# Performance work log

Measured on AMD Instinct MI355X. Metric: run time of the kernel, lower is better.

## Reference

```python
import jax, jax.numpy as jnp
import numpy as np

D = 1024
H = 16
DH = D // H  # 64
EPS_LN = 1e-5
CONF_MIN = 1e-6


def sparsemax(z):
    """Sparsemax along the last axis (Martins & Astudillo 2016)."""
    K = z.shape[-1]
    z_sorted = jnp.flip(jnp.sort(z, axis=-1), axis=-1)          # descending
    cssv = jnp.cumsum(z_sorted, axis=-1)                        # cumulative sums
    r = jnp.arange(1, K + 1, dtype=z.dtype)                     # 1..K
    support = (1.0 + r * z_sorted) > cssv                       # bool mask
    k = jnp.sum(support, axis=-1, keepdims=True)                # support size
    tau = (jnp.take_along_axis(cssv, k.astype(jnp.int32) - 1, axis=-1) - 1.0) / k.astype(z.dtype)
    return jnp.maximum(z - tau, 0.0)


def setup_inputs() -> dict:
    key = jax.random.key(0)
    ks = jax.random.split(key, 16)
    B, P, K = 8, 512, 16
    s = 0.02
    return {
        "cell_query": jax.random.normal(ks[0], (B, D), jnp.float32),
        "gene_facets": jax.random.normal(ks[1], (B, P, K, D), jnp.float32),
        "confidence": jax.random.uniform(ks[2], (B, P, K), jnp.float32),
        "wq": jax.random.normal(ks[3], (D, D), jnp.float32) * s,
        "bq": jnp.zeros((D,), jnp.float32),
        "wk": jax.random.normal(ks[4], (D, D), jnp.float32) * s,
        "bk": jnp.zeros((D,), jnp.float32),
        "wv": jax.random.normal(ks[5], (D, D), jnp.float32) * s,
        "bv": jnp.zeros((D,), jnp.float32),
        "wo": jax.random.normal(ks[6], (D, D), jnp.float32) * s,
        "bo": jnp.zeros((D,), jnp.float32),
        "gamma": jnp.ones((D,), jnp.float32),
        "beta": jnp.zeros((D,), jnp.float32),
    }


def reference(cell_query, gene_facets, confidence,
              wq, bq, wk, bk, wv, bv, wo, bo, gamma, beta):
    B = gene_facets.shape[0]
    P = gene_facets.shape[1]
    Kf = gene_facets.shape[2]

    # Projections (torch Linear: x @ W^T + b; here weights stored already transposed as (D,D))
    Q = (cell_query @ wq + bq).reshape(B, H, DH)                       # (B,H,d)
    Kp = (gene_facets @ wk + bk).reshape(B, P, Kf, H, DH)              # (B,P,K,H,d)
    Vp = (gene_facets @ wv + bv).reshape(B, P, Kf, H, DH)              # (B,P,K,H,d)

    # scores: (B,P,H,K)
    scores = jnp.einsum('bhd,bpkhd->bphk', Q, Kp) / jnp.sqrt(jnp.asarray(DH, Q.dtype))
    conf_bias = jnp.log(jnp.clip(confidence, CONF_MIN))                # (B,P,K)
    scores = scores + conf_bias[:, :, None, :]

    alpha = sparsemax(scores)                                          # (B,P,H,K), dropout_p=0 -> identity

    out = jnp.einsum('bphk,bpkhd->bphd', alpha, Vp).reshape(B, P, D)
    out = out @ wo + bo

    # LayerNorm over last dim
    mu = jnp.mean(out, axis=-1, keepdims=True)
    var = jnp.mean((out - mu) ** 2, axis=-1, keepdims=True)
    out = (out - mu) * jax.lax.rsqrt(var + EPS_LN) * gamma + beta
    return out, alpha
```

## Files before the change

### kernel.cpp

```cpp
#include <hip/hip_runtime.h>


typedef float f32x4 __attribute__((ext_vector_type(4)));
typedef short s16x4 __attribute__((ext_vector_type(4)));
typedef short s16x8 __attribute__((ext_vector_type(8)));

__device__ __forceinline__ unsigned short f2bf(float f) {
  unsigned u = __builtin_bit_cast(unsigned, f);
  u = (u + 0x7FFFu + ((u >> 16) & 1u)) >> 16;
  return (unsigned short)u;
}

__device__ __forceinline__ float bf2f(unsigned short u) {
  return __builtin_bit_cast(float, ((unsigned)u) << 16);
}

__device__ __forceinline__ s16x8 pack8(s16x4 lo, s16x4 hi) {
  s16x8 r;
  r[0] = lo[0]; r[1] = lo[1]; r[2] = lo[2]; r[3] = lo[3];
  r[4] = hi[0]; r[5] = hi[1]; r[6] = hi[2]; r[7] = hi[3];
  return r;
}

__global__ __launch_bounds__(256) void k_transq(
    const float* __restrict__ wv, const float* __restrict__ wo,
    unsigned short* __restrict__ wvt, unsigned short* __restrict__ wot,
    const float* __restrict__ cq, const float* __restrict__ wq,
    float* __restrict__ qpart) {
  int bid = blockIdx.x;
  int t = threadIdx.x;
  if (bid < 512) {
    __shared__ float ts[64][65];
    const float* src = (bid < 256) ? wv : wo;
    unsigned short* dst = (bid < 256) ? wvt : wot;
    int tile = bid & 255;
    int er = (tile >> 4) << 6;
    int cb = (tile & 15) << 6;
    int r = t >> 2, c0 = (t & 3) << 4;
#pragma unroll
    for (int j = 0; j < 16; j += 4) {
      f32x4 v = *(const f32x4*)&src[(long)(er + r) * 1024 + cb + c0 + j];
      ts[r][c0 + j + 0] = v[0];
      ts[r][c0 + j + 1] = v[1];
      ts[r][c0 + j + 2] = v[2];
      ts[r][c0 + j + 3] = v[3];
    }
    __syncthreads();
    s16x8 o0, o1;
#pragma unroll
    for (int j = 0; j < 8; ++j) o0[j] = (short)f2bf(ts[c0 + j][r]);
#pragma unroll
    for (int j = 0; j < 8; ++j) o1[j] = (short)f2bf(ts[c0 + 8 + j][r]);
    long ob = (long)(cb + r) * 1024 + er + c0;
    *(s16x8*)&dst[ob] = o0;
    *(s16x8*)&dst[ob + 8] = o1;
  } else {
    int idx = bid - 512;
    int eq = idx >> 2, dq = idx & 3;
    int d = (dq << 8) + t;
    float acc[8] = {};
    for (int i = 0; i < 64; ++i) {
      int e = (eq << 6) + i;
      float w = wq[(long)e * 1024 + d];
#pragma unroll
      for (int b = 0; b < 8; ++b) acc[b] += w * cq[(b << 10) + e];
    }
#pragma unroll
    for (int b = 0; b < 8; ++b)
      qpart[(long)((b << 4) + eq) * 1024 + d] = acc[b];
  }
}

__global__ __launch_bounds__(256) void k_wtilde(
    const float* __restrict__ wk, const float* __restrict__ bk,
    const float* __restrict__ bq, const float* __restrict__ qpart,
    unsigned short* __restrict__ wt, float* __restrict__ cvec) {
  __shared__ float Qs[16][68];
  int et = blockIdx.x, b = blockIdx.y, t = threadIdx.x;
  {
    int d0 = t << 2;
    f32x4 s4 = *(const f32x4*)&bq[d0];
#pragma unroll
    for (int q = 0; q < 16; ++q)
      s4 += *(const f32x4*)&qpart[(long)((b << 4) + q) * 1024 + d0];
    *(f32x4*)&Qs[d0 >> 6][d0 & 63] = s4;
  }
  __syncthreads();
  int h = t & 15, el = t >> 4;
#pragma unroll
  for (int ii = 0; ii < 2; ++ii) {
    int e = (et << 5) + (ii << 4) + el;
    const float* wr = &wk[(long)e * 1024 + (h << 6)];
    float s = 0.f;
#pragma unroll
    for (int d = 0; d < 64; d += 4) {
      f32x4 w = *(const f32x4*)&wr[d];
      s += w[0] * Qs[h][d] + w[1] * Qs[h][d + 1] + w[2] * Qs[h][d + 2] + w[3] * Qs[h][d + 3];
    }
    wt[(long)((b << 4) + h) * 1024 + e] = f2bf(s);
  }
  if (et == 0 && t < 16) {
    float s = 0.f;
    for (int d = 0; d < 64; ++d) s += bk[(t << 6) + d] * Qs[t][d];
    cvec[(b << 4) + t] = s;
  }
}

#define GSTR 1028
#define TSTR 20
__global__ __launch_bounds__(256, 2) void k_scores(
    const float* __restrict__ G, const float* __restrict__ conf,
    const unsigned short* __restrict__ wt, const float* __restrict__ cvec,
    float* __restrict__ alpha_out, unsigned short* __restrict__ gbar,
    int b0, int hstride) {
  __shared__ short Gs[16 * GSTR];
  __shared__ short Gt[1024 * TSTR];
  __shared__ short As[16 * 32];
  __shared__ float ps[1024];
  __shared__ float lc[16];

  int t = threadIdx.x;
  int lane = t & 63, w = t >> 6;
  int l15 = lane & 15, g4 = lane >> 4;
  int bp = blockIdx.x;
  long gbp = (long)b0 * 512 + bp;
  int b = (int)(gbp >> 9);
  const float* Grow = G + gbp * 16384;
  const unsigned short* wtb = wt + (long)b * 16384;

#pragma unroll
  for (int half = 0; half < 2; ++half) {
    s16x4 col[8];
#pragma unroll
    for (int j = 0; j < 8; ++j) {
      int k = (half << 3) + j;
      f32x4 g = *(const f32x4*)&Grow[(k << 10) + (t << 2)];
      s16x4 h4;
      h4[0] = (short)f2bf(g[0]); h4[1] = (short)f2bf(g[1]);
      h4[2] = (short)f2bf(g[2]); h4[3] = (short)f2bf(g[3]);
      *(s16x4*)&Gs[k * GSTR + (t << 2)] = h4;
      col[j] = h4;
    }
#pragma unroll
    for (int q = 0; q < 4; ++q) {
      int e = (t << 2) + q;
      s16x4 lo, hi;
      lo[0] = col[0][q]; lo[1] = col[1][q]; lo[2] = col[2][q]; lo[3] = col[3][q];
      hi[0] = col[4][q]; hi[1] = col[5][q]; hi[2] = col[6][q]; hi[3] = col[7][q];
      *(s16x4*)&Gt[e * TSTR + (half << 3)] = lo;
      *(s16x4*)&Gt[e * TSTR + (half << 3) + 4] = hi;
    }
  }
  if (t < 16) lc[t] = logf(fmaxf(conf[gbp * 16 + t], 1e-6f));
  __syncthreads();

  f32x4 sc = {0.f, 0.f, 0.f, 0.f};
#pragma unroll
  for (int i = 0; i < 8; ++i) {
    int e0 = (w << 8) + (i << 5) + (g4 << 3);
    s16x8 af = *(const s16x8*)&wtb[l15 * 1024 + e0];
    int off = l15 * GSTR + e0;
    s16x8 bf = pack8(*(const s16x4*)&Gs[off], *(const s16x4*)&Gs[off + 4]);
    sc = __builtin_amdgcn_mfma_f32_16x16x32_bf16(af, bf, sc, 0, 0, 0);
  }
#pragma unroll
  for (int r = 0; r < 4; ++r)
    ps[(w << 8) + ((g4 << 2) + r) * 16 + l15] = sc[r];
  __syncthreads();

  {
    int h = t >> 4, k = t & 15;
    float z = (ps[h * 16 + k] + ps[256 + h * 16 + k] + ps[512 + h * 16 + k] +
               ps[768 + h * 16 + k] + cvec[b * 16 + h]) * 0.125f + lc[k];
    float v = z;
#pragma unroll
    for (int kk = 2; kk <= 16; kk <<= 1) {
#pragma unroll
      for (int j = kk >> 1; j > 0; j >>= 1) {
        float o = __shfl_xor(v, j, 64);
        bool dirDesc = ((l15 & kk) == 0);
        bool takeMax = (((l15 & j) == 0) == dirDesc);
        v = takeMax ? fmaxf(v, o) : fminf(v, o);
      }
    }
    float cs = v;
#pragma unroll
    for (int d = 1; d < 16; d <<= 1) {
      float o = __shfl_up(cs, (unsigned)d, 16);
      if (l15 >= d) cs += o;
    }
    bool sup = (1.0f + (float)(l15 + 1) * v) > cs;
    unsigned long long m = __ballot(sup);
    int gb16 = lane & 48;
    int ksup = (int)__popcll((m >> gb16) & 0xFFFFull);
    float csk = __shfl(cs, ksup - 1, 16);
    float tau = (csk - 1.0f) / (float)ksup;
    float a = fmaxf(z - tau, 0.0f);
    alpha_out[((gbp << 4) + h) * 16 + k] = a;
    As[(h << 5) + k] = (short)f2bf(a);
    As[(h << 5) + 16 + k] = 0;
  }
  __syncthreads();

  s16x8 ab = *(const s16x8*)&As[(l15 << 5) + (g4 << 3)];
#pragma unroll 4
  for (int i = 0; i < 16; ++i) {
    int ebase = ((w << 4) + i) << 4;
    int ro = (ebase + l15) * TSTR + ((g4 & 1) << 3);
    s16x8 aa = pack8(*(const s16x4*)&Gt[ro], *(const s16x4*)&Gt[ro + 4]);
    f32x4 d2 = __builtin_amdgcn_mfma_f32_16x16x32_bf16(
        aa, ab, (f32x4){0.f, 0.f, 0.f, 0.f}, 0, 0, 0);
    s16x4 o4;
    o4[0] = (short)f2bf(d2[0]); o4[1] = (short)f2bf(d2[1]);
    o4[2] = (short)f2bf(d2[2]); o4[3] = (short)f2bf(d2[3]);
    *(s16x4*)&gbar[(long)l15 * hstride + (long)bp * 1024 + ebase + (g4 << 2)] = o4;
  }
}

__global__ __launch_bounds__(256) void k_av(
    const unsigned short* __restrict__ gbar, const unsigned short* __restrict__ wvt,
    const float* __restrict__ bv, unsigned short* __restrict__ av,
    int b0, int hstride) {
  __shared__ short Asm[64 * 40];
  __shared__ short Bsm[64 * 40];
  int t = threadIdx.x;
  int lane = t & 63, w = t >> 6;
  int l15 = lane & 15, g4 = lane >> 4;
  int wm = w >> 1, wn = w & 1;
  int tile = blockIdx.x, h = blockIdx.y;
  const unsigned short* Ab = gbar + (long)h * hstride + (long)tile * 64 * 1024;
  const unsigned short* Bb = wvt + (long)(h << 6) * 1024;
  int lr = t >> 2, lc = (t & 3) << 3;
  const unsigned short* Arp = Ab + (long)lr * 1024 + lc;
  const unsigned short* Brp = Bb + (long)lr * 1024 + lc;
  s16x8 a8 = *(const s16x8*)&Arp[0];
  s16x8 b8 = *(const s16x8*)&Brp[0];
  f32x4 acc[2][2] = {};
  for (int kb = 0; kb < 32; ++kb) {
    __syncthreads();
    *(s16x8*)&Asm[lr * 40 + lc] = a8;
    *(s16x8*)&Bsm[lr * 40 + lc] = b8;
    if (kb + 1 < 32) {
      a8 = *(const s16x8*)&Arp[((kb + 1) << 5)];
      b8 = *(const s16x8*)&Brp[((kb + 1) << 5)];
    }
    __syncthreads();
    s16x8 afr[2], bfr[2];
#pragma unroll
    for (int im = 0; im < 2; ++im)
      afr[im] = *(const s16x8*)&Asm[(wm * 32 + im * 16 + l15) * 40 + (g4 << 3)];
#pragma unroll
    for (int in = 0; in < 2; ++in)
      bfr[in] = *(const s16x8*)&Bsm[(wn * 32 + in * 16 + l15) * 40 + (g4 << 3)];
#pragma unroll
    for (int im = 0; im < 2; ++im)
#pragma unroll
      for (int in = 0; in < 2; ++in)
        acc[im][in] = __builtin_amdgcn_mfma_f32_16x16x32_bf16(afr[im], bfr[in], acc[im][in], 0, 0, 0);
  }
  long grow0 = (long)b0 * 512 + (long)tile * 64 + wm * 32 + (g4 << 2);
#pragma unroll
  for (int in = 0; in < 2; ++in) {
    int colg = (h << 6) + wn * 32 + in * 16 + l15;
    float bvv = bv[colg];
#pragma unroll
    for (int im = 0; im < 2; ++im) {
      long rowg = grow0 + im * 16;
#pragma unroll
      for (int r = 0; r < 4; ++r)
        av[(rowg + r) * 1024 + colg] = f2bf(acc[im][in][r] + bvv);
    }
  }
}

__global__ __launch_bounds__(256) void k_out(
    const unsigned short* __restrict__ av, const unsigned short* __restrict__ wot,
    const float* __restrict__ bo, unsigned short* __restrict__ yb) {
  __shared__ short Asm[64 * 40];
  __shared__ short Bsm[64 * 40];
  int mt = blockIdx.x, nt = blockIdx.y, t = threadIdx.x;
  int lane = t & 63, w = t >> 6;
  int wm = w >> 1, wn = w & 1;
  int l15 = lane & 15, g4 = lane >> 4;
  int lr = t >> 2, lc = (t & 3) << 3;
  const unsigned short* Arp = av + (long)(mt * 64 + lr) * 1024 + lc;
  const unsigned short* Brp = wot + (long)(nt * 64 + lr) * 1024 + lc;
  s16x8 a8 = *(const s16x8*)&Arp[0];
  s16x8 b8 = *(const s16x8*)&Brp[0];
  f32x4 acc[2][2] = {};
  for (int kb = 0; kb < 32; ++kb) {
    __syncthreads();
    *(s16x8*)&Asm[lr * 40 + lc] = a8;
    *(s16x8*)&Bsm[lr * 40 + lc] = b8;
    if (kb + 1 < 32) {
      a8 = *(const s16x8*)&Arp[((kb + 1) << 5)];
      b8 = *(const s16x8*)&Brp[((kb + 1) << 5)];
    }
    __syncthreads();
    s16x8 afr[2], bfr[2];
#pragma unroll
    for (int im = 0; im < 2; ++im)
      afr[im] = *(const s16x8*)&Asm[(wm * 32 + im * 16 + l15) * 40 + (g4 << 3)];
#pragma unroll
    for (int in = 0; in < 2; ++in)
      bfr[in] = *(const s16x8*)&Bsm[(wn * 32 + in * 16 + l15) * 40 + (g4 << 3)];
#pragma unroll
    for (int im = 0; im < 2; ++im)
#pragma unroll
      for (int in = 0; in < 2; ++in)
        acc[im][in] = __builtin_amdgcn_mfma_f32_16x16x32_bf16(afr[im], bfr[in], acc[im][in], 0, 0, 0);
  }
#pragma unroll
  for (int in = 0; in < 2; ++in) {
    int colg = nt * 64 + wn * 32 + in * 16 + l15;
    float bov = bo[colg];
#pragma unroll
    for (int im = 0; im < 2; ++im) {
      long rowg = (long)mt * 64 + wm * 32 + im * 16 + (g4 << 2);
#pragma unroll
      for (int r = 0; r < 4; ++r)
        yb[(rowg + r) * 1024 + colg] = f2bf(acc[im][in][r] + bov);
    }
  }
}

__global__ __launch_bounds__(256) void k_ln(
    const unsigned short* __restrict__ yb, const float* __restrict__ gamma,
    const float* __restrict__ beta, float* __restrict__ y) {
  int row = (blockIdx.x << 2) + (threadIdx.x >> 6);
  int lane = threadIdx.x & 63;
  const unsigned short* yr = yb + ((long)row << 10);
  float v[4][4];
  float s = 0.f, s2 = 0.f;
#pragma unroll
  for (int j = 0; j < 4; ++j) {
    s16x4 h4 = *(const s16x4*)&yr[(lane << 2) + (j << 8)];
#pragma unroll
    for (int q = 0; q < 4; ++q) {
      float f = bf2f((unsigned short)h4[q]);
      v[j][q] = f; s += f; s2 += f * f;
    }
  }
#pragma unroll
  for (int d = 1; d < 64; d <<= 1) {
    s += __shfl_xor(s, d, 64);
    s2 += __shfl_xor(s2, d, 64);
  }
  float mu = s * (1.0f / 1024.0f);
  float var = s2 * (1.0f / 1024.0f) - mu * mu;
  float rs = rsqrtf(var + 1e-5f);
  float* yo = y + ((long)row << 10);
#pragma unroll
  for (int j = 0; j < 4; ++j) {
    int f0 = (lane << 2) + (j << 8);
    f32x4 gm = *(const f32x4*)&gamma[f0];
    f32x4 bt = *(const f32x4*)&beta[f0];
    f32x4 o;
#pragma unroll
    for (int q = 0; q < 4; ++q) o[q] = (v[j][q] - mu) * rs * gm[q] + bt[q];
    *(f32x4*)&yo[f0] = o;
  }
}

extern "C" void kernel_launch(void* const* d_in, const int* in_sizes, int n_in,
                              void* d_out, int out_size, void* d_ws, size_t ws_size,
                              hipStream_t stream) {
  (void)in_sizes; (void)n_in; (void)out_size;
  const float* cq    = (const float*)d_in[0];
  const float* G     = (const float*)d_in[1];
  const float* conf  = (const float*)d_in[2];
  const float* wq    = (const float*)d_in[3];
  const float* bq    = (const float*)d_in[4];
  const float* wk    = (const float*)d_in[5];
  const float* bk    = (const float*)d_in[6];
  const float* wv    = (const float*)d_in[7];
  const float* bv    = (const float*)d_in[8];
  const float* wo    = (const float*)d_in[9];
  const float* bo    = (const float*)d_in[10];
  const float* gamma = (const float*)d_in[11];
  const float* beta  = (const float*)d_in[12];

  float* y = (float*)d_out;
  float* alpha = y + 4194304;

  char* p = (char*)d_ws;
  float* qpart = (float*)p;                  p += 8L * 16 * 1024 * 4;
  float* cvec  = (float*)p;                  p += 1024;
  unsigned short* wt   = (unsigned short*)p; p += 8L * 16 * 1024 * 2;
  unsigned short* wvt  = (unsigned short*)p; p += 1024L * 1024 * 2;
  unsigned short* wot  = (unsigned short*)p; p += 1024L * 1024 * 2;
  unsigned short* av   = (unsigned short*)p; p += 4096L * 1024 * 2;
  unsigned short* yb   = (unsigned short*)p; p += 4096L * 1024 * 2;
  unsigned short* gbar = (unsigned short*)p;
  size_t used = (size_t)(p - (char*)d_ws);
  size_t per_b = 512L * 16 * 1024 * 2;
  int nb = 1;
  if (ws_size >= used + 8 * per_b) nb = 8;
  else if (ws_size >= used + 4 * per_b) nb = 4;
  else if (ws_size >= used + 2 * per_b) nb = 2;
  int hstride = nb * 512 * 1024;

  hipLaunchKernelGGL(k_transq, dim3(576), dim3(256), 0, stream,
                     wv, wo, wvt, wot, cq, wq, qpart);
  hipLaunchKernelGGL(k_wtilde, dim3(32, 8), dim3(256), 0, stream, wk, bk, bq, qpart, wt, cvec);
  for (int c = 0; c < 8; c += nb) {
    hipLaunchKernelGGL(k_scores, dim3(nb * 512), dim3(256), 0, stream,
                       G, conf, wt, cvec, alpha, gbar, c, hstride);
    hipLaunchKernelGGL(k_av, dim3(nb * 8, 16), dim3(256), 0, stream,
                       gbar, wvt, bv, av, c, hstride);
  }
  hipLaunchKernelGGL(k_out, dim3(64, 16), dim3(256), 0, stream, av, wot, bo, yb);
  hipLaunchKernelGGL(k_ln, dim3(1024), dim3(256), 0, stream, yb, gamma, beta, y);
}
```

Baseline: 201.5 us.

## Stage gbar through LDS for coalesced stores, halve k_av tile, cap batch chunk at 4

k_scores now writes its per-head weighted facet sums into a shared-memory buffer (Gs) and then stores them to global memory as contiguous 16-byte vectors, replacing the scattered 8-byte per-lane stores. k_av uses 32-row M tiles instead of 64, which doubles its grid to give more blocks per launch. The batch chunk size is capped at 4, so the workspace footprint shrinks and there are two score/av launch pairs. The tradeoff is an extra LDS round trip and barrier in k_scores, less reuse per k_av block, and extra launches.

```diff
diff --git a/kernel.cpp b/kernel.cpp
--- a/kernel.cpp
+++ b/kernel.cpp
@@ -213,7 +213,18 @@
     s16x4 o4;
     o4[0] = (short)f2bf(d2[0]); o4[1] = (short)f2bf(d2[1]);
     o4[2] = (short)f2bf(d2[2]); o4[3] = (short)f2bf(d2[3]);
-    *(s16x4*)&gbar[(long)l15 * hstride + (long)bp * 1024 + ebase + (g4 << 2)] = o4;
+    *(s16x4*)&Gs[l15 * GSTR + ebase + (g4 << 2)] = o4;
+  }
+  __syncthreads();
+
+  unsigned short* gbo = gbar + (long)bp * 1024;
+#pragma unroll
+  for (int c2 = 0; c2 < 8; ++c2) {
+    int flat = (c2 << 11) + (t << 3);
+    int hh = flat >> 10, e = flat & 1023;
+    s16x4 lo = *(const s16x4*)&Gs[hh * GSTR + e];
+    s16x4 hi = *(const s16x4*)&Gs[hh * GSTR + e + 4];
+    *(s16x8*)&gbo[(long)hh * hstride + e] = pack8(lo, hi);
   }
 }
 
@@ -221,55 +232,48 @@
     const unsigned short* __restrict__ gbar, const unsigned short* __restrict__ wvt,
     const float* __restrict__ bv, unsigned short* __restrict__ av,
     int b0, int hstride) {
-  __shared__ short Asm[64 * 40];
+  __shared__ short Asm[32 * 40];
   __shared__ short Bsm[64 * 40];
   int t = threadIdx.x;
   int lane = t & 63, w = t >> 6;
   int l15 = lane & 15, g4 = lane >> 4;
   int wm = w >> 1, wn = w & 1;
   int tile = blockIdx.x, h = blockIdx.y;
-  const unsigned short* Ab = gbar + (long)h * hstride + (long)tile * 64 * 1024;
+  const unsigned short* Ab = gbar + (long)h * hstride + (long)tile * 32 * 1024;
   const unsigned short* Bb = wvt + (long)(h << 6) * 1024;
-  int lr = t >> 2, lc = (t & 3) << 3;
-  const unsigned short* Arp = Ab + (long)lr * 1024 + lc;
-  const unsigned short* Brp = Bb + (long)lr * 1024 + lc;
-  s16x8 a8 = *(const s16x8*)&Arp[0];
+  int ar = t >> 3, ac = (t & 7) << 2;
+  int br = t >> 2, bc = (t & 3) << 3;
+  const unsigned short* Arp = Ab + (long)ar * 1024 + ac;
+  const unsigned short* Brp = Bb + (long)br * 1024 + bc;
+  s16x4 a4 = *(const s16x4*)&Arp[0];
   s16x8 b8 = *(const s16x8*)&Brp[0];
-  f32x4 acc[2][2] = {};
+  f32x4 acc[2] = {};
   for (int kb = 0; kb < 32; ++kb) {
     __syncthreads();
-    *(s16x8*)&Asm[lr * 40 + lc] = a8;
-    *(s16x8*)&Bsm[lr * 40 + lc] = b8;
+    *(s16x4*)&Asm[ar * 40 + ac] = a4;
+    *(s16x8*)&Bsm[br * 40 + bc] = b8;
     if (kb + 1 < 32) {
-      a8 = *(const s16x8*)&Arp[((kb + 1) << 5)];
+      a4 = *(const s16x4*)&Arp[((kb + 1) << 5)];
       b8 = *(const s16x8*)&Brp[((kb + 1) << 5)];
     }
     __syncthreads();
-    s16x8 afr[2], bfr[2];
-#pragma unroll
-    for (int im = 0; im < 2; ++im)
-      afr[im] = *(const s16x8*)&Asm[(wm * 32 + im * 16 + l15) * 40 + (g4 << 3)];
+    s16x8 afr = *(const s16x8*)&Asm[(wm * 16 + l15) * 40 + (g4 << 3)];
+    s16x8 bfr[2];
 #pragma unroll
     for (int in = 0; in < 2; ++in)
       bfr[in] = *(const s16x8*)&Bsm[(wn * 32 + in * 16 + l15) * 40 + (g4 << 3)];
 #pragma unroll
-    for (int im = 0; im < 2; ++im)
-#pragma unroll
-      for (int in = 0; in < 2; ++in)
-        acc[im][in] = __builtin_amdgcn_mfma_f32_16x16x32_bf16(afr[im], bfr[in], acc[im][in], 0, 0, 0);
-  }
-  long grow0 = (long)b0 * 512 + (long)tile * 64 + wm * 32 + (g4 << 2);
+    for (int in = 0; in < 2; ++in)
+      acc[in] = __builtin_amdgcn_mfma_f32_16x16x32_bf16(afr, bfr[in], acc[in], 0, 0, 0);
+  }
+  long grow0 = (long)b0 * 512 + (long)tile * 32 + wm * 16 + (g4 << 2);
 #pragma unroll
   for (int in = 0; in < 2; ++in) {
     int colg = (h << 6) + wn * 32 + in * 16 + l15;
     float bvv = bv[colg];
 #pragma unroll
-    for (int im = 0; im < 2; ++im) {
-      long rowg = grow0 + im * 16;
-#pragma unroll
-      for (int r = 0; r < 4; ++r)
-        av[(rowg + r) * 1024 + colg] = f2bf(acc[im][in][r] + bvv);
-    }
+    for (int r = 0; r < 4; ++r)
+      av[(grow0 + r) * 1024 + colg] = f2bf(acc[in][r] + bvv);
   }
 }
 
@@ -395,8 +399,7 @@
   size_t used = (size_t)(p - (char*)d_ws);
   size_t per_b = 512L * 16 * 1024 * 2;
   int nb = 1;
-  if (ws_size >= used + 8 * per_b) nb = 8;
-  else if (ws_size >= used + 4 * per_b) nb = 4;
+  if (ws_size >= used + 4 * per_b) nb = 4;
   else if (ws_size >= used + 2 * per_b) nb = 2;
   int hstride = nb * 512 * 1024;
 
@@ -406,7 +409,7 @@
   for (int c = 0; c < 8; c += nb) {
     hipLaunchKernelGGL(k_scores, dim3(nb * 512), dim3(256), 0, stream,
                        G, conf, wt, cvec, alpha, gbar, c, hstride);
-    hipLaunchKernelGGL(k_av, dim3(nb * 8, 16), dim3(256), 0, stream,
+    hipLaunchKernelGGL(k_av, dim3(nb * 16, 16), dim3(256), 0, stream,
                        gbar, wvt, bv, av, c, hstride);
   }
   hipLaunchKernelGGL(k_out, dim3(64, 16), dim3(256), 0, stream, av, wot, bo, yb);
```

Result: faster. 188.3 us (-6.5%).
